# Kernel tuning notes

Hardware: AMD Instinct MI355X
Metric: run time of the kernel (lower is better)

The kernel has to match this reference:

```python
import jax, jax.numpy as jnp
import numpy as np


def _relative_position_index(ws: int) -> np.ndarray:
    # Same construction as in the Keras layer __init__ (Swin-style).
    coords = np.stack(np.meshgrid(np.arange(ws), np.arange(ws), indexing='ij'))  # (2, ws, ws)
    coords = coords.reshape(2, -1)                                               # (2, N)
    rel = coords[:, :, None] - coords[:, None, :]                                # (2, N, N)
    rel = rel.transpose(1, 2, 0)                                                 # (N, N, 2)
    idx = (rel[..., 0] + ws - 1) * (2 * ws - 1) + (rel[..., 1] + ws - 1)         # (N, N)
    return idx.astype(np.int32)


def setup_inputs() -> dict:
    key = jax.random.key(0)
    kx, kw, kb, kp, kpb, kt = jax.random.split(key, 6)
    B, N, dim = 128, 240, 512
    ws, H = 16, 16
    s_in = (1.0 / np.sqrt(dim)).astype(np.float32)
    x = jax.random.normal(kx, (B, N, dim), dtype=jnp.float32)
    qkv_w = jax.random.normal(kw, (dim, 3 * dim), dtype=jnp.float32) * s_in
    qkv_b = jnp.zeros((3 * dim,), dtype=jnp.float32)
    proj_w = jax.random.normal(kp, (dim, dim), dtype=jnp.float32) * s_in
    proj_b = jnp.zeros((dim,), dtype=jnp.float32)
    rel_bias_table = jax.random.normal(kt, ((2 * ws - 1) ** 2, H), dtype=jnp.float32) * 0.02
    return {
        'x': x,
        'qkv_w': qkv_w,
        'qkv_b': qkv_b,
        'proj_w': proj_w,
        'proj_b': proj_b,
        'rel_bias_table': rel_bias_table,
        'window_size': ws,
    }


def reference(x, qkv_w, qkv_b, proj_w, proj_b, rel_bias_table, window_size):
    B, N, dim = x.shape
    H = rel_bias_table.shape[1]
    head_dim = dim // H
    scale = head_dim ** -0.5
    Np = window_size * window_size
    pad = Np - N

    # --- internal padding to window_size^2 tokens ---
    xp = jnp.pad(x, ((0, 0), (0, pad), (0, 0)))  # (B, Np, dim)

    # --- joint QKV projection ---
    qkv = xp @ qkv_w + qkv_b                                   # (B, Np, 3*dim)
    qkv = qkv.reshape(B, Np, 3, H, head_dim)
    qkv = jnp.transpose(qkv, (2, 0, 3, 1, 4))                  # (3, B, H, Np, hd)
    q, k, v = qkv[0], qkv[1], qkv[2]

    # --- scaled dot-product scores + relative position bias ---
    attn = jnp.einsum('bhqd,bhkd->bhqk', q, k) * scale         # (B, H, Np, Np)
    rel_idx = jnp.asarray(_relative_position_index(window_size))
    bias = rel_bias_table[rel_idx]                             # (Np, Np, H)
    attn = attn + jnp.transpose(bias, (2, 0, 1))[None]

    # --- padding mask on key positions ---
    key_valid = jnp.arange(Np) < N                             # (Np,)
    attn = jnp.where(key_valid[None, None, None, :], attn, jnp.float32(-1e9))

    # --- softmax normalization ---
    attn = jax.nn.softmax(attn, axis=-1)

    # --- weighted sum over values ---
    out = jnp.einsum('bhqk,bhkd->bhqd', attn, v)               # (B, H, Np, hd)
    out = jnp.transpose(out, (0, 2, 1, 3)).reshape(B, Np, dim)

    # --- output projection and unpad ---
    out = out @ proj_w + proj_b
    return out[:, :N, :]
```

## Files before the change

kernel.cpp:

```cpp
#include <hip/hip_runtime.h>
#include <hip/hip_bf16.h>

typedef __attribute__((ext_vector_type(8))) short bf16x8;
typedef __attribute__((ext_vector_type(4))) short s16x4;
typedef __attribute__((ext_vector_type(2))) int i32x2;
typedef __attribute__((ext_vector_type(4))) float f32x4;

__device__ __forceinline__ short f2bf(float f) {
  unsigned u = __builtin_bit_cast(unsigned, f);
  u = (u + 0x7FFFu + ((u >> 16) & 1u)) >> 16;
  return (short)u;
}

__device__ __forceinline__ void gload_lds16(const void* g, void* l) {
  __builtin_amdgcn_global_load_lds(
      (const __attribute__((address_space(1))) void*)g,
      (__attribute__((address_space(3))) void*)l, 16, 0, 0);
}

__device__ __forceinline__ f32x4 mfma16(s16x4 a, s16x4 b, f32x4 c) {
#if __has_builtin(__builtin_amdgcn_mfma_f32_16x16x16bf16_1k)
  return __builtin_amdgcn_mfma_f32_16x16x16bf16_1k(a, b, c, 0, 0, 0);
#else
  asm("v_mfma_f32_16x16x16_bf16 %0, %1, %2, %0" : "+v"(c) : "v"(a), "v"(b));
  return c;
#endif
}

#define SBAR()       asm volatile("s_barrier" ::: "memory")
#define WAIT_VM4()   asm volatile("s_waitcnt vmcnt(4)" ::: "memory")
#define WAIT_VM0()   asm volatile("s_waitcnt vmcnt(0)" ::: "memory")
#define WAIT_LGKM0() asm volatile("s_waitcnt lgkmcnt(0)" ::: "memory")

__global__ void k_prep(const float* __restrict__ x, const float* __restrict__ qkv_w,
                       const float* __restrict__ proj_w, const float* __restrict__ table,
                       short* __restrict__ xb, short* __restrict__ qkv_wt,
                       short* __restrict__ proj_wt, float* __restrict__ expB) {
  const int bid = blockIdx.x;
  if (bid < 15360) {
    int i = bid * 256 + threadIdx.x;
    const float4 v = *(const float4*)(x + (size_t)i * 4);
    s16x4 o;
    o.x = f2bf(v.x); o.y = f2bf(v.y); o.z = f2bf(v.z); o.w = f2bf(v.w);
    *(s16x4*)(xb + (size_t)i * 4) = o;
  } else if (bid < 18432) {
    int i = (bid - 15360) * 256 + threadIdx.x;
    int k = i & 511, n = i >> 9;
    qkv_wt[i] = f2bf(qkv_w[(size_t)k * 1536 + n]);
  } else if (bid < 19456) {
    int i = (bid - 18432) * 256 + threadIdx.x;
    int k = i & 511, n = i >> 9;
    proj_wt[i] = f2bf(proj_w[(size_t)k * 512 + n]);
  } else {
    int i = (bid - 19456) * 256 + threadIdx.x;
    int lane = i & 63;
    int rest = i >> 6;
    int j = rest % 15;
    int hq = rest / 15;
    int q = (hq & 15) * 16 + (lane & 15);
    int h = hq >> 4;
    int kbase = j * 16 + ((lane >> 4) << 2);
    float4 o;
    float* op = &o.x;
#pragma unroll
    for (int r = 0; r < 4; ++r) {
      int k = kbase + r;
      int idx = ((q >> 4) - (k >> 4) + 15) * 31 + ((q & 15) - (k & 15) + 15);
      op[r] = __builtin_amdgcn_exp2f(table[idx * 16 + h] * 1.4426950408889634f);
    }
    *(float4*)(expB + (size_t)i * 4) = o;
  }
}

template <int MODE, int NBN>
__global__ __launch_bounds__(512, 2)
void k_gemm(const short* __restrict__ A, const short* __restrict__ Bt,
            const float* __restrict__ bias,
            short* __restrict__ qo, short* __restrict__ ko, short* __restrict__ vo,
            float* __restrict__ fo) {
  __shared__ alignas(16) short lds[2][32][512];
  const int lane = threadIdx.x & 63;
  const int w = threadIdx.x >> 6;
  const int wm = w >> 2;
  const int wn = w & 3;
  const int arow = lane & 15;
  const int g = lane >> 4;
  const int kc8 = g * 8;

  const int nwg = 120 * NBN;
  const int bid = blockIdx.x;
  const int swz = (bid & 7) * (nwg >> 3) + (bid >> 3);
  const int nb = swz % NBN, mc = swz / NBN;
  const int n0 = nb * 256, m0 = mc * 256;

  const short* gsrc[4];
#pragma unroll
  for (int s = 0; s < 4; ++s) {
    const int t = w * 4 + s;
    gsrc[s] = (t < 16 ? A + (size_t)(m0 + t * 16 + arow) * 512
                      : Bt + (size_t)(n0 + (t - 16) * 16 + arow) * 512) + kc8;
  }

#define STAGE(buf, k0)                                       \
  {                                                          \
    _Pragma("unroll")                                        \
    for (int s = 0; s < 4; ++s)                              \
      gload_lds16(gsrc[s] + (k0), &lds[buf][w * 4 + s][0]);  \
  }

  float bv[4];
#pragma unroll
  for (int j = 0; j < 4; ++j) bv[j] = bias[n0 + wn * 64 + j * 16 + arow];

  f32x4 acc[8][4] = {};
  STAGE(0, 0);
  STAGE(1, 32);
#pragma unroll
  for (int kt = 0; kt < 16; ++kt) {
    const int cur = kt & 1;
    if (kt < 15) WAIT_VM4(); else WAIT_VM0();
    SBAR();
    bf16x8 af[8], bfr[4];
#pragma unroll
    for (int i = 0; i < 8; ++i)
      af[i] = *(const bf16x8*)&lds[cur][wm * 8 + i][lane * 8];
#pragma unroll
    for (int j = 0; j < 4; ++j)
      bfr[j] = *(const bf16x8*)&lds[cur][16 + wn * 4 + j][lane * 8];
#pragma unroll
    for (int i = 0; i < 8; ++i)
#pragma unroll
      for (int j = 0; j < 4; ++j)
        acc[i][j] = __builtin_amdgcn_mfma_f32_16x16x32_bf16(af[i], bfr[j], acc[i][j], 0, 0, 0);
    WAIT_LGKM0();
    __builtin_amdgcn_sched_barrier(0);
    SBAR();
    if (kt < 14) STAGE(cur, (kt + 2) * 32);
  }
#undef STAGE

  const float sc = 0.17677669529663687f * 1.4426950408889634f;
  if (MODE == 0) {
    const int part = n0 >> 9;
    short* dst = part == 0 ? qo : (part == 1 ? ko : vo);
    const float osc = part == 0 ? sc : 1.f;
    if (part != 1) {
#pragma unroll
      for (int i = 0; i < 8; ++i) {
        const int mm0 = m0 + wm * 128 + i * 16 + g * 4;
        const int bb = mm0 / 240, tt0 = mm0 - bb * 240;
#pragma unroll
        for (int j = 0; j < 4; ++j) {
          const int c = n0 + wn * 64 + j * 16 + arow;
          const int d = c & 31, hh = (c >> 5) & 15;
          s16x4 qv;
#pragma unroll
          for (int r = 0; r < 4; ++r)
            qv[r] = f2bf((acc[i][j][r] + bv[j]) * osc);
          *(s16x4*)(dst + ((size_t)(bb * 16 + hh) * 32 + d) * 240 + tt0) = qv;
        }
      }
    } else {
#pragma unroll
      for (int i = 0; i < 8; ++i) {
        const int mm0 = m0 + wm * 128 + i * 16 + g * 4;
        const int bb = mm0 / 240, tt0 = mm0 - bb * 240;
#pragma unroll
        for (int j = 0; j < 4; ++j) {
          const int c = n0 + wn * 64 + j * 16 + arow;
          const int d = c & 31, hh = (c >> 5) & 15;
#pragma unroll
          for (int r = 0; r < 4; ++r)
            dst[((size_t)(bb * 16 + hh) * 240 + tt0 + r) * 32 + d] =
                f2bf(acc[i][j][r] + bv[j]);
        }
      }
    }
  } else {
#pragma unroll
    for (int i = 0; i < 8; ++i) {
      const int mm0 = m0 + wm * 128 + i * 16 + g * 4;
#pragma unroll
      for (int j = 0; j < 4; ++j) {
        const int c = n0 + wn * 64 + j * 16 + arow;
#pragma unroll
        for (int r = 0; r < 4; ++r)
          fo[(size_t)(mm0 + r) * 512 + c] = acc[i][j][r] + bv[j];
      }
    }
  }
}

__global__ __launch_bounds__(512, 4)
void k_attn(const short* __restrict__ Qg, const short* __restrict__ Kg,
            const short* __restrict__ Vg, const float* __restrict__ expB,
            short* __restrict__ O) {
  __shared__ alignas(16) short ldsK[15 * 512];
  __shared__ alignas(16) short ldsVT[32 * 264];
  const int lane = threadIdx.x & 63;
  const int w = threadIdx.x >> 6;
  const int bh = blockIdx.x;
  const int h = bh & 15, b = bh >> 4;
  const short* Qb = Qg + (size_t)bh * 7680;
  const short* Kb = Kg + (size_t)bh * 7680;
  const short* Vb = Vg + (size_t)bh * 7680;
  const int arow = lane & 15;
  const int g = lane >> 4;

#pragma unroll
  for (int kt = 0; kt < 15; ++kt)
    if ((kt & 7) == w)
      gload_lds16(Kb + (kt * 16 + arow) * 32 + g * 8, &ldsK[kt * 512]);

  for (int c2 = threadIdx.x; c2 < 960; c2 += 512) {
    int d = c2 / 30, tc = c2 - d * 30;
    *(bf16x8*)&ldsVT[d * 264 + tc * 8] = *(const bf16x8*)(Vb + d * 240 + tc * 8);
  }

  bf16x8 qf[2];
#pragma unroll
  for (int i = 0; i < 2; ++i) {
    if (w * 2 + i < 15) {
#pragma unroll
      for (int e = 0; e < 8; ++e)
        qf[i][e] = Qb[(g * 8 + e) * 240 + (w * 2 + i) * 16 + arow];
    }
  }
  __syncthreads();

  const f32x4 zf = {0.f, 0.f, 0.f, 0.f};
#pragma unroll
  for (int qt = 0; qt < 2; ++qt) {
    const int qtile = w * 2 + qt;
    if (qtile >= 15) continue;
    f32x4 sacc[15];
#pragma unroll
    for (int j = 0; j < 15; ++j) {
      bf16x8 kf = *(const bf16x8*)&ldsK[j * 512 + lane * 8];
      sacc[j] = __builtin_amdgcn_mfma_f32_16x16x32_bf16(kf, qf[qt], zf, 0, 0, 0);
    }
    float m = fmaxf(fmaxf(sacc[0][0], sacc[0][1]), fmaxf(sacc[0][2], sacc[0][3]));
#pragma unroll
    for (int j = 1; j < 15; ++j)
      m = fmaxf(m, fmaxf(fmaxf(sacc[j][0], sacc[j][1]), fmaxf(sacc[j][2], sacc[j][3])));
    m = fmaxf(m, __shfl_xor(m, 16));
    m = fmaxf(m, __shfl_xor(m, 32));
    const float* ebp = expB + (size_t)((h * 16 + qtile) * 15) * 256 + lane * 4;
    float sum = 0.f;
    s16x4 pa[15];
#pragma unroll
    for (int j = 0; j < 15; ++j) {
      float4 eb = *(const float4*)(ebp + j * 256);
      float p0 = __builtin_amdgcn_exp2f(sacc[j][0] - m) * eb.x;
      float p1 = __builtin_amdgcn_exp2f(sacc[j][1] - m) * eb.y;
      float p2 = __builtin_amdgcn_exp2f(sacc[j][2] - m) * eb.z;
      float p3 = __builtin_amdgcn_exp2f(sacc[j][3] - m) * eb.w;
      sum += (p0 + p1) + (p2 + p3);
      i32x2 pk;
      asm("v_cvt_pk_bf16_f32 %0, %1, %2" : "=v"(pk.x) : "v"(p0), "v"(p1));
      asm("v_cvt_pk_bf16_f32 %0, %1, %2" : "=v"(pk.y) : "v"(p2), "v"(p3));
      pa[j] = __builtin_bit_cast(s16x4, pk);
    }
    sum += __shfl_xor(sum, 16);
    sum += __shfl_xor(sum, 32);
    float rs = __builtin_amdgcn_rcpf(sum);
    float rsr[4];
#pragma unroll
    for (int r = 0; r < 4; ++r)
      rsr[r] = __shfl(rs, (lane & 48) + ((lane & 48) >> 2) + r, 64);
    f32x4 oacc[2] = {};
#pragma unroll
    for (int j = 0; j < 15; ++j) {
#pragma unroll
      for (int dt = 0; dt < 2; ++dt) {
        s16x4 vt = *(const s16x4*)&ldsVT[(dt * 16 + arow) * 264 + j * 16 + g * 4];
        oacc[dt] = mfma16(pa[j], vt, oacc[dt]);
      }
    }
    const int q0 = qtile * 16;
#pragma unroll
    for (int dt = 0; dt < 2; ++dt)
#pragma unroll
      for (int r = 0; r < 4; ++r)
        O[(size_t)(b * 240 + q0 + 4 * g + r) * 512 + h * 32 + dt * 16 + arow] =
            f2bf(oacc[dt][r] * rsr[r]);
  }
}


extern "C" void kernel_launch(void* const* d_in, const int* in_sizes, int n_in,
                              void* d_out, int out_size, void* d_ws, size_t ws_size,
                              hipStream_t stream) {
  const float* x      = (const float*)d_in[0];
  const float* qkv_w  = (const float*)d_in[1];
  const float* qkv_b  = (const float*)d_in[2];
  const float* proj_w = (const float*)d_in[3];
  const float* proj_b = (const float*)d_in[4];
  const float* table  = (const float*)d_in[5];
  float* out = (float*)d_out;

  char* ws = (char*)d_ws;
  short* xb      = (short*)(ws);
  short* Qg      = (short*)(ws + 33554432u);
  short* Kg      = (short*)(ws + 67108864u);
  short* Vg      = (short*)(ws + 100663296u);
  float* expBf   = (float*)(ws + 134217728u);
  short* qkv_wt  = (short*)(ws + 138412032u);
  short* proj_wt = (short*)(ws + 139984896u);

  k_prep<<<20416, 256, 0, stream>>>(x, qkv_w, proj_w, table, xb, qkv_wt, proj_wt, expBf);
  k_gemm<0, 6><<<720, 512, 0, stream>>>(xb, qkv_wt, qkv_b, Qg, Kg, Vg, nullptr);
  k_attn<<<2048, 512, 0, stream>>>(Qg, Kg, Vg, expBf, xb);
  k_gemm<1, 2><<<240, 512, 0, stream>>>(xb, proj_wt, proj_b, nullptr, nullptr, nullptr, out);
}
```

Measured before the change: 157.4 us.

## Deepen GEMM LDS pipeline to four half-stages with split MFMA phases

Restructures the bf16 GEMM main loop so LDS holds two 64-wide k-tiles, each split into two 32-wide halves, giving four staged loads in flight instead of two. Each half-step issues half its MFMAs, then refills the freed buffer, then issues the rest, so global-to-LDS loads overlap with compute. MFMA blocks are raised in priority with s_setprio. Doubling LDS to 128 KB forces launch bounds down to one workgroup per CU, which lowers occupancy and hides less latency across workgroups.

```diff
diff --git a/kernel.cpp b/kernel.cpp
--- a/kernel.cpp
+++ b/kernel.cpp
@@ -28,6 +28,8 @@
 }
 
 #define SBAR()       asm volatile("s_barrier" ::: "memory")
+#define WAIT_VM12()  asm volatile("s_waitcnt vmcnt(12)" ::: "memory")
+#define WAIT_VM8()   asm volatile("s_waitcnt vmcnt(8)" ::: "memory")
 #define WAIT_VM4()   asm volatile("s_waitcnt vmcnt(4)" ::: "memory")
 #define WAIT_VM0()   asm volatile("s_waitcnt vmcnt(0)" ::: "memory")
 #define WAIT_LGKM0() asm volatile("s_waitcnt lgkmcnt(0)" ::: "memory")
@@ -73,12 +75,12 @@
 }
 
 template <int MODE, int NBN>
-__global__ __launch_bounds__(512, 2)
+__global__ __launch_bounds__(512, 1)
 void k_gemm(const short* __restrict__ A, const short* __restrict__ Bt,
             const float* __restrict__ bias,
             short* __restrict__ qo, short* __restrict__ ko, short* __restrict__ vo,
             float* __restrict__ fo) {
-  __shared__ alignas(16) short lds[2][32][512];
+  __shared__ alignas(16) short lds[2][2][32][512];
   const int lane = threadIdx.x & 63;
   const int w = threadIdx.x >> 6;
   const int wm = w >> 2;
@@ -93,19 +95,18 @@
   const int nb = swz % NBN, mc = swz / NBN;
   const int n0 = nb * 256, m0 = mc * 256;
 
-  const short* gsrc[4];
-#pragma unroll
-  for (int s = 0; s < 4; ++s) {
-    const int t = w * 4 + s;
-    gsrc[s] = (t < 16 ? A + (size_t)(m0 + t * 16 + arow) * 512
-                      : Bt + (size_t)(n0 + (t - 16) * 16 + arow) * 512) + kc8;
-  }
-
-#define STAGE(buf, k0)                                       \
-  {                                                          \
-    _Pragma("unroll")                                        \
-    for (int s = 0; s < 4; ++s)                              \
-      gload_lds16(gsrc[s] + (k0), &lds[buf][w * 4 + s][0]);  \
+  const short* aS0 = A + (size_t)(m0 + (2 * w) * 16 + arow) * 512 + kc8;
+  const short* aS1 = A + (size_t)(m0 + (2 * w + 1) * 16 + arow) * 512 + kc8;
+  const short* bS0 = Bt + (size_t)(n0 + (2 * w) * 16 + arow) * 512 + kc8;
+  const short* bS1 = Bt + (size_t)(n0 + (2 * w + 1) * 16 + arow) * 512 + kc8;
+
+#define STG(buf, kh, kt)                                          \
+  {                                                               \
+    const int kof = (kt) * 64 + (kh) * 32;                        \
+    gload_lds16(aS0 + kof, &lds[buf][kh][2 * w][0]);              \
+    gload_lds16(aS1 + kof, &lds[buf][kh][2 * w + 1][0]);          \
+    gload_lds16(bS0 + kof, &lds[buf][kh][16 + 2 * w][0]);         \
+    gload_lds16(bS1 + kof, &lds[buf][kh][16 + 2 * w + 1][0]);     \
   }
 
   float bv[4];
@@ -113,31 +114,65 @@
   for (int j = 0; j < 4; ++j) bv[j] = bias[n0 + wn * 64 + j * 16 + arow];
 
   f32x4 acc[8][4] = {};
-  STAGE(0, 0);
-  STAGE(1, 32);
-#pragma unroll
-  for (int kt = 0; kt < 16; ++kt) {
-    const int cur = kt & 1;
-    if (kt < 15) WAIT_VM4(); else WAIT_VM0();
-    SBAR();
-    bf16x8 af[8], bfr[4];
-#pragma unroll
-    for (int i = 0; i < 8; ++i)
-      af[i] = *(const bf16x8*)&lds[cur][wm * 8 + i][lane * 8];
-#pragma unroll
-    for (int j = 0; j < 4; ++j)
-      bfr[j] = *(const bf16x8*)&lds[cur][16 + wn * 4 + j][lane * 8];
-#pragma unroll
-    for (int i = 0; i < 8; ++i)
+  STG(0, 0, 0); STG(0, 1, 0); STG(1, 0, 1); STG(1, 1, 1);
+  WAIT_VM12();
+  SBAR();
+
+#pragma unroll
+  for (int t = 0; t < 8; ++t) {
+    const int cb = t & 1;
+    bf16x8 a[8], b[4];
+#pragma unroll
+    for (int i = 0; i < 8; ++i) a[i] = *(const bf16x8*)&lds[cb][0][wm * 8 + i][lane * 8];
+#pragma unroll
+    for (int j = 0; j < 4; ++j) b[j] = *(const bf16x8*)&lds[cb][0][16 + wn * 4 + j][lane * 8];
+    __builtin_amdgcn_s_setprio(1);
+#pragma unroll
+    for (int i = 0; i < 4; ++i)
 #pragma unroll
       for (int j = 0; j < 4; ++j)
-        acc[i][j] = __builtin_amdgcn_mfma_f32_16x16x32_bf16(af[i], bfr[j], acc[i][j], 0, 0, 0);
+        acc[i][j] = __builtin_amdgcn_mfma_f32_16x16x32_bf16(a[i], b[j], acc[i][j], 0, 0, 0);
+    __builtin_amdgcn_s_setprio(0);
     WAIT_LGKM0();
     __builtin_amdgcn_sched_barrier(0);
     SBAR();
-    if (kt < 14) STAGE(cur, (kt + 2) * 32);
-  }
-#undef STAGE
+    if (t < 6) STG(cb, 0, t + 2);
+    __builtin_amdgcn_s_setprio(1);
+#pragma unroll
+    for (int i = 4; i < 8; ++i)
+#pragma unroll
+      for (int j = 0; j < 4; ++j)
+        acc[i][j] = __builtin_amdgcn_mfma_f32_16x16x32_bf16(a[i], b[j], acc[i][j], 0, 0, 0);
+    __builtin_amdgcn_s_setprio(0);
+    if (t <= 5) { WAIT_VM12(); } else if (t == 6) { WAIT_VM8(); } else { WAIT_VM0(); }
+    SBAR();
+    bf16x8 a2[8], b2[4];
+#pragma unroll
+    for (int i = 0; i < 8; ++i) a2[i] = *(const bf16x8*)&lds[cb][1][wm * 8 + i][lane * 8];
+#pragma unroll
+    for (int j = 0; j < 4; ++j) b2[j] = *(const bf16x8*)&lds[cb][1][16 + wn * 4 + j][lane * 8];
+    __builtin_amdgcn_s_setprio(1);
+#pragma unroll
+    for (int i = 0; i < 4; ++i)
+#pragma unroll
+      for (int j = 0; j < 4; ++j)
+        acc[i][j] = __builtin_amdgcn_mfma_f32_16x16x32_bf16(a2[i], b2[j], acc[i][j], 0, 0, 0);
+    __builtin_amdgcn_s_setprio(0);
+    WAIT_LGKM0();
+    __builtin_amdgcn_sched_barrier(0);
+    SBAR();
+    if (t < 6) STG(cb, 1, t + 2);
+    __builtin_amdgcn_s_setprio(1);
+#pragma unroll
+    for (int i = 4; i < 8; ++i)
+#pragma unroll
+      for (int j = 0; j < 4; ++j)
+        acc[i][j] = __builtin_amdgcn_mfma_f32_16x16x32_bf16(a2[i], b2[j], acc[i][j], 0, 0, 0);
+    __builtin_amdgcn_s_setprio(0);
+    if (t <= 5) { WAIT_VM12(); } else if (t == 6) { WAIT_VM4(); }
+    SBAR();
+  }
+#undef STG
 
   const float sc = 0.17677669529663687f * 1.4426950408889634f;
   if (MODE == 0) {
```

Result: no change. 158.9 us (+1.0%).
